# Optimization experiments

Measured on AMD Instinct MI355X. Metric: run time of the kernel, lower is better.

## Reference

```python
import jax, jax.numpy as jnp
from jax import lax
import numpy as np

G, K = 8, 9  # deformable groups, 3x3 kernel taps


def conv1x1_bn_relu(x, W, scale, bias):
    # Conv2d 1x1 (no bias) + folded eval-mode BatchNorm (per-channel scale/bias) + ReLU
    y = jnp.einsum('bchw,oc->bohw', x, W)
    return jax.nn.relu(y * scale[None, :, None, None] + bias[None, :, None, None])


def dcn_v2(feat, offset_feat, W_om, b_om, W_dcn, b_dcn):
    # Modulated deformable conv v2, 3x3, stride 1, pad 1, dilation 1,
    # deformable_groups=G, extra_offset_mask: offsets/mask predicted from offset_feat.
    B, C, H, W_ = feat.shape
    Cg = C // G
    om = lax.conv_general_dilated(offset_feat, W_om, (1, 1), ((1, 1), (1, 1)))
    om = om + b_om[None, :, None, None]              # [B, 3*G*K, H, W]
    o1, o2, m = jnp.split(om, 3, axis=1)
    off_y = o1.reshape(B, G, K, H, W_)
    off_x = o2.reshape(B, G, K, H, W_)
    mask = jax.nn.sigmoid(m).reshape(B, G, K, H, W_)
    dk = jnp.arange(3) - 1
    dkh = jnp.repeat(dk, 3)   # tap row offset,  k = kh*3 + kw
    dkw = jnp.tile(dk, 3)     # tap col offset
    hh = jnp.arange(H, dtype=feat.dtype)
    ww = jnp.arange(W_, dtype=feat.dtype)
    py = hh[None, None, None, :, None] + dkh[None, None, :, None, None].astype(feat.dtype) + off_y
    px = ww[None, None, None, None, :] + dkw[None, None, :, None, None].astype(feat.dtype) + off_x
    y0 = jnp.floor(py); x0 = jnp.floor(px)
    ty = py - y0; tx = px - x0
    xg = feat.reshape(B, G, Cg, H * W_)

    def gather(idx):  # idx [B,G,K,H,W] int32 -> [B,G,Cg,K,H,W]
        f = lambda xf, i: xf[:, i]
        return jax.vmap(jax.vmap(f))(xg, idx)

    val = jnp.zeros((B, G, Cg, K, H, W_), dtype=feat.dtype)
    y0i = y0.astype(jnp.int32); x0i = x0.astype(jnp.int32)
    for dy, wy in ((0, 1.0 - ty), (1, ty)):
        iy = y0i + dy
        vy = (iy >= 0) & (iy < H)
        iyc = jnp.clip(iy, 0, H - 1)
        for dx, wx in ((0, 1.0 - tx), (1, tx)):
            ix = x0i + dx
            v = vy & (ix >= 0) & (ix < W_)
            idx = iyc * W_ + jnp.clip(ix, 0, W_ - 1)
            w = (wy * wx) * v.astype(feat.dtype)      # zero-padding outside
            val = val + w[:, :, None] * gather(idx)
    val = val * mask[:, :, None]                      # modulation
    Wd = W_dcn.reshape(W_dcn.shape[0], G, Cg, K)      # [Cout, G, Cg, K]
    out = jnp.einsum('bgckhw,ogck->bohw', val, Wd) + b_dcn[None, :, None, None]
    return out


def setup_inputs() -> dict:
    key = jax.random.key(0)
    ks = jax.random.split(key, 16)
    B, C, H, W_ = 8, 128, 64, 64
    Cd = C // 2  # dcn out channels = 64
    d = {}
    d['feat_l'] = jax.random.normal(ks[0], (B, C, H, W_), jnp.float32)
    d['feat_s'] = jax.random.normal(ks[1], (B, C, H // 2, W_ // 2), jnp.float32)
    d['W_fsm'] = jax.random.normal(ks[2], (C, C), jnp.float32) / np.sqrt(C)
    d['s_fsm'] = 1.0 + 0.1 * jax.random.normal(ks[3], (C,), jnp.float32)
    d['b_fsm'] = 0.1 * jax.random.normal(ks[4], (C,), jnp.float32)
    d['W_off'] = jax.random.normal(ks[5], (C, 2 * C), jnp.float32) / np.sqrt(2 * C)
    d['s_off'] = 1.0 + 0.1 * jax.random.normal(ks[6], (C,), jnp.float32)
    d['b_off'] = 0.1 * jax.random.normal(ks[7], (C,), jnp.float32)
    d['W_om'] = 0.05 * jax.random.normal(ks[8], (3 * G * K, C, 3, 3), jnp.float32)
    d['b_om'] = jnp.zeros((3 * G * K,), jnp.float32)
    d['W_dcn'] = jax.random.normal(ks[9], (Cd, C, 3, 3), jnp.float32) / np.sqrt(C * 9)
    d['b_dcn'] = 0.1 * jax.random.normal(ks[10], (Cd,), jnp.float32)
    d['W_cat'] = jax.random.normal(ks[11], (C, Cd), jnp.float32) / np.sqrt(Cd)
    d['s_cat'] = 1.0 + 0.1 * jax.random.normal(ks[12], (C,), jnp.float32)
    d['b_cat'] = 0.1 * jax.random.normal(ks[13], (C,), jnp.float32)
    return d


def reference(feat_l, feat_s, W_fsm, s_fsm, b_fsm, W_off, s_off, b_off,
              W_om, b_om, W_dcn, b_dcn, W_cat, s_cat, b_cat):
    # nearest upsample x2 (F.interpolate nearest to feat_l spatial size)
    feat_up = jnp.repeat(jnp.repeat(feat_s, 2, axis=2), 2, axis=3)
    feat_arm = conv1x1_bn_relu(feat_l, W_fsm, s_fsm, b_fsm)
    offset = conv1x1_bn_relu(jnp.concatenate([feat_arm, feat_up * 2.0], axis=1),
                             W_off, s_off, b_off)
    feat_align = jax.nn.relu(dcn_v2(feat_up, offset, W_om, b_om, W_dcn, b_dcn))
    feat = conv1x1_bn_relu(feat_align, W_cat, s_cat, b_cat) + feat_arm
    return (feat, feat_arm)
```

## Files before the change

kernel.cpp:

```cpp
#include <hip/hip_runtime.h>


typedef __attribute__((ext_vector_type(8))) short short8;
typedef __attribute__((ext_vector_type(4))) float f32x4;
typedef __attribute__((ext_vector_type(16))) float f32x16;
typedef _Float16 __attribute__((ext_vector_type(2))) h2;

union F16u { f32x16 v; f32x4 q[4]; };

static __device__ __forceinline__ unsigned short f2bf(float x) {
    union { float f; unsigned int u; } v; v.f = x;
    return (unsigned short)((v.u + 0x7FFF + ((v.u >> 16) & 1)) >> 16);
}
static __device__ __forceinline__ unsigned short f2h(float x) {
    union { _Float16 h; unsigned short u; } v; v.h = (_Float16)x;
    return v.u;
}

__global__ __launch_bounds__(256) void k_prep(const float* __restrict__ fs,
        uint4* __restrict__ fsT4, uint4* __restrict__ fsC4,
        const float* __restrict__ W_fsm, const float* __restrict__ W_off,
        const float* __restrict__ W_cat, const float* __restrict__ W_dcn,
        const float* __restrict__ W_om,
        unsigned short* __restrict__ wbfsm, unsigned short* __restrict__ wboff,
        unsigned short* __restrict__ wbcat, unsigned short* __restrict__ wbdcn,
        unsigned short* __restrict__ wb2) {
    __shared__ unsigned short st[64 * 136];
    const int t = threadIdx.x;
    if (blockIdx.x < 128) {
        unsigned int* st32 = (unsigned int*)st;
        const int b = blockIdx.x >> 4;
        const int p0 = (blockIdx.x & 15) << 6;
        for (int i = t; i < 64 * 64; i += 256) {
            int c2 = i >> 6, px = i & 63;
            float v0 = fs[(((b << 7) + 2 * c2) << 10) + p0 + px];
            float v1 = fs[(((b << 7) + 2 * c2 + 1) << 10) + p0 + px];
            st32[px * 68 + c2] = (unsigned int)f2bf(v0) | ((unsigned int)f2bf(v1) << 16);
        }
        __syncthreads();
        for (int i = t; i < 64 * 16; i += 256) {
            int px = i >> 4, q = i & 15;
            fsT4[(((b << 10) + p0 + px) << 4) + q] = ((const uint4*)(st + px * 136))[q];
        }
        __syncthreads();
        for (int i = t; i < 64 * 64; i += 256) {
            int c2 = i >> 6, px = i & 63;
            float v0 = fs[(((b << 7) + 2 * c2) << 10) + p0 + px];
            float v1 = fs[(((b << 7) + 2 * c2 + 1) << 10) + p0 + px];
            st32[px * 68 + c2] = (unsigned int)f2h(v0) | ((unsigned int)f2h(v1) << 16);
        }
        __syncthreads();
        for (int i = t; i < 64 * 16; i += 256) {
            int ci = i >> 6, px = i & 63;
            fsC4[(b << 14) + (ci << 10) + p0 + px] = ((const uint4*)(st + px * 136))[ci];
        }
        return;
    }
    int idx = (blockIdx.x - 128) * 256 + t;
    int lane = idx & 63;
    int ml = lane & 15, kl = (lane >> 4) * 8;
    unsigned short tmp[8];
    if (idx < 2048) {
        int r = idx >> 6;
        int o = (r % 8) * 16 + ml, k0 = (r / 8) * 32 + kl;
#pragma unroll
        for (int j = 0; j < 8; j++) tmp[j] = f2bf(W_fsm[o * 128 + k0 + j]);
        ((uint4*)wbfsm)[idx] = *(const uint4*)tmp;
    } else if (idx < 6144) {
        int i2 = idx - 2048;
        int r = i2 >> 6;
        int o = (r % 8) * 16 + ml, k0 = (r / 8) * 32 + kl;
#pragma unroll
        for (int j = 0; j < 8; j++) {
            int k = k0 + j;
            float f = W_off[o * 256 + k];
            if (k >= 128) f *= 2.0f;
            tmp[j] = f2bf(f);
        }
        ((uint4*)wboff)[i2] = *(const uint4*)tmp;
    } else if (idx < 7168) {
        int i2 = idx - 6144;
        int r = i2 >> 6;
        int o = (r % 8) * 16 + ml, k0 = (r / 8) * 32 + kl;
#pragma unroll
        for (int j = 0; j < 8; j++) tmp[j] = f2bf(W_cat[o * 64 + k0 + j]);
        ((uint4*)wbcat)[i2] = *(const uint4*)tmp;
    } else if (idx < 16384) {
        int i2 = idx - 7168;
        int r = i2 >> 6;
        int o = (r & 1) * 32 + (lane & 31);
        int k0 = (r >> 1) * 16 + (lane >> 5) * 8;
#pragma unroll
        for (int j = 0; j < 8; j++) {
            int k = k0 + j;
            int g = k / 144;
            int rem = k - g * 144;
            tmp[j] = f2h(W_dcn[(o * 128 + g * 16 + (rem & 15)) * 9 + (rem >> 4)]);
        }
        ((uint4*)wbdcn)[i2] = *(const uint4*)tmp;
    } else if (idx < 48640) {
        int i2 = idx - 16384;
        int r = i2 >> 6;
        int nt = r % 14, kk = r / 14;
        int tap = kk >> 2, cc = kk & 3;
        int o = nt * 16 + ml;
        int c0 = cc * 32 + kl;
#pragma unroll
        for (int j = 0; j < 8; j++) {
            float v = (o < 216) ? W_om[(o * 128 + (c0 + j)) * 9 + tap] : 0.0f;
            tmp[j] = f2bf(v);
        }
        ((uint4*)wb2)[i2] = *(const uint4*)tmp;
    }
}

__global__ __launch_bounds__(512, 6) void k12(const float* __restrict__ feat_l,
        const uint4* __restrict__ fsT4,
        const unsigned short* __restrict__ wbf, const unsigned short* __restrict__ wbo,
        const float* __restrict__ s_fsm, const float* __restrict__ b_fsm,
        const float* __restrict__ s_off, const float* __restrict__ b_off,
        float* __restrict__ feat_arm, unsigned short* __restrict__ offT) {
    __shared__ unsigned short A1[64 * 136];
    __shared__ unsigned short A2[64 * 264];
    const int t = threadIdx.x;
    const int b = blockIdx.x >> 6;
    const int h = blockIdx.x & 63;
    const int hw0 = h << 6;
    unsigned int* A1w = (unsigned int*)A1;
    for (int i = t; i < 64 * 64; i += 512) {
        int c2 = i >> 6, px = i & 63;
        float v0 = feat_l[(((b << 7) + 2 * c2) << 12) + hw0 + px];
        float v1 = feat_l[(((b << 7) + 2 * c2 + 1) << 12) + hw0 + px];
        A1w[px * 68 + c2] = (unsigned int)f2bf(v0) | ((unsigned int)f2bf(v1) << 16);
    }
    {
        const int h2 = h >> 1;
        int px2 = t >> 4, q = t & 15;
        uint4 v = fsT4[(((b << 10) + (h2 << 5) + px2) << 4) + q];
        ((uint4*)(A2 + (2 * px2) * 264 + 128))[q] = v;
        ((uint4*)(A2 + (2 * px2 + 1) * 264 + 128))[q] = v;
    }
    __syncthreads();
    const int lane = t & 63;
    const int w = __builtin_amdgcn_readfirstlane(t >> 6);
    const int ph = w & 1;
    const int nq4 = w >> 1;
    const int m = lane & 15, ko = lane >> 4;
    f32x4 acc[2][2];
#pragma unroll
    for (int i = 0; i < 2; i++)
#pragma unroll
        for (int j = 0; j < 2; j++) acc[i][j] = (f32x4){0.f, 0.f, 0.f, 0.f};
#pragma unroll
    for (int kk = 0; kk < 4; kk++) {
        short8 a8[2];
#pragma unroll
        for (int mt = 0; mt < 2; mt++)
            a8[mt] = *(const short8*)(A1 + ((ph << 5) + (mt << 4) + m) * 136 + kk * 32 + ko * 8);
#pragma unroll
        for (int nt2 = 0; nt2 < 2; nt2++) {
            uint4 bu = ((const uint4*)wbf)[((kk << 3) + (nq4 << 1) + nt2) * 64 + lane];
#pragma unroll
            for (int mt = 0; mt < 2; mt++)
                acc[mt][nt2] = __builtin_amdgcn_mfma_f32_16x16x32_bf16(
                    a8[mt], *(short8*)&bu, acc[mt][nt2], 0, 0, 0);
        }
    }
#pragma unroll
    for (int nt2 = 0; nt2 < 2; nt2++) {
        int o = (((nq4 << 1) + nt2) << 4) + m;
        float sc = s_fsm[o], bi = b_fsm[o];
#pragma unroll
        for (int mt = 0; mt < 2; mt++) {
            int px0 = (ph << 5) + (mt << 4) + (ko << 2);
            f32x4 v;
#pragma unroll
            for (int r = 0; r < 4; r++) {
                float vv = fmaf(acc[mt][nt2][r], sc, bi);
                vv = vv > 0.f ? vv : 0.f;
                v[r] = vv;
                A2[(px0 + r) * 264 + o] = f2bf(vv);
            }
            *(f32x4*)(feat_arm + ((((b << 7) + o) << 12) + hw0 + px0)) = v;
        }
    }
    __syncthreads();
    f32x4 acc2[2][2];
#pragma unroll
    for (int i = 0; i < 2; i++)
#pragma unroll
        for (int j = 0; j < 2; j++) acc2[i][j] = (f32x4){0.f, 0.f, 0.f, 0.f};
#pragma unroll
    for (int kk = 0; kk < 8; kk++) {
        short8 a8[2];
#pragma unroll
        for (int mt = 0; mt < 2; mt++)
            a8[mt] = *(const short8*)(A2 + ((ph << 5) + (mt << 4) + m) * 264 + kk * 32 + ko * 8);
#pragma unroll
        for (int nt2 = 0; nt2 < 2; nt2++) {
            uint4 bu = ((const uint4*)wbo)[((kk << 3) + (nq4 << 1) + nt2) * 64 + lane];
#pragma unroll
            for (int mt = 0; mt < 2; mt++)
                acc2[mt][nt2] = __builtin_amdgcn_mfma_f32_16x16x32_bf16(
                    a8[mt], *(short8*)&bu, acc2[mt][nt2], 0, 0, 0);
        }
    }
    __syncthreads();
#pragma unroll
    for (int nt2 = 0; nt2 < 2; nt2++) {
        int o = (((nq4 << 1) + nt2) << 4) + m;
        float sc = s_off[o], bi = b_off[o];
#pragma unroll
        for (int mt = 0; mt < 2; mt++) {
            int px0 = (ph << 5) + (mt << 4) + (ko << 2);
#pragma unroll
            for (int r = 0; r < 4; r++) {
                float v = fmaf(acc2[mt][nt2][r], sc, bi);
                v = v > 0.f ? v : 0.f;
                A2[(px0 + r) * 264 + o] = f2bf(v);
            }
        }
    }
    __syncthreads();
    for (int i = t; i < 64 * 16; i += 512) {
        int px = i >> 4, q = i & 15;
        ((uint4*)offT)[(((b << 12) + hw0 + px) << 4) + q] = ((const uint4*)(A2 + px * 264))[q];
    }
}

__global__ __launch_bounds__(512, 4) void k_omdcn(
        const unsigned short* __restrict__ offT, const uint4* __restrict__ fsC4,
        const unsigned short* __restrict__ Wb2, const float* __restrict__ bom,
        const unsigned short* __restrict__ wbd, const float* __restrict__ bd,
        const unsigned short* __restrict__ wbc,
        const float* __restrict__ s_cat, const float* __restrict__ b_cat,
        const float* __restrict__ feat_arm, float* __restrict__ feat) {
    __shared__ float LDSf[13464];
    unsigned short* st = (unsigned short*)LDSf;
    float* oyL = LDSf;
    float* oxL = LDSf + 4672;
    unsigned short* mskL = (unsigned short*)(LDSf + 9344);
    float* Rbuf = LDSf;
    unsigned short* A3 = (unsigned short*)(LDSf + 9216);
    const uint4* offT4 = (const uint4*)offT;
    const uint4* W4 = (const uint4*)Wb2;
    const uint4* wbd4 = (const uint4*)wbd;
    const int t = threadIdx.x;
    const int b = blockIdx.x >> 6;
    const int h = blockIdx.x & 63;
    for (int i = t; i < 3 * 66 * 16; i += 512) {
        int q = i & 15;
        int rp = i >> 4;
        int r = rp / 66, p = rp - r * 66;
        int gy = h + r - 1, gx = p - 1;
        uint4 v = make_uint4(0, 0, 0, 0);
        if (gy >= 0 && gy < 64 && gx >= 0 && gx < 64)
            v = offT4[((((b << 6) + gy) << 6) + gx) * 16 + q];
        ((uint4*)(st + rp * 136))[q] = v;
    }
    __syncthreads();
    const int lane = t & 63;
    const int w = __builtin_amdgcn_readfirstlane(t >> 6);
    const int m = lane & 15, ko = lane >> 4;
    f32x4 acc[2][4];
#pragma unroll
    for (int i = 0; i < 2; i++)
#pragma unroll
        for (int j = 0; j < 4; j++) acc[i][j] = (f32x4){0.f, 0.f, 0.f, 0.f};
    if (w < 7) {
        const int ntb = w << 1;
        uint4 b4c[2];
#pragma unroll
        for (int nt2 = 0; nt2 < 2; nt2++)
            b4c[nt2] = W4[((ntb + nt2) << 6) + lane];
#pragma unroll
        for (int kk = 0; kk < 36; kk++) {
            const int tap = kk >> 2, cc = kk & 3;
            const int dy = tap / 3, dx = tap - dy * 3;
            uint4 b4n[2];
            if (kk < 35) {
#pragma unroll
                for (int nt2 = 0; nt2 < 2; nt2++)
                    b4n[nt2] = W4[(((kk + 1) * 14 + ntb + nt2) << 6) + lane];
            }
            short8 a8[4];
#pragma unroll
            for (int mt = 0; mt < 4; mt++) {
                int p = mt * 16 + m + dx;
                a8[mt] = *(const short8*)(st + (dy * 66 + p) * 136 + (cc << 5) + (ko << 3));
            }
            __builtin_amdgcn_s_setprio(1);
#pragma unroll
            for (int nt2 = 0; nt2 < 2; nt2++)
#pragma unroll
                for (int mt = 0; mt < 4; mt++)
                    acc[nt2][mt] = __builtin_amdgcn_mfma_f32_16x16x32_bf16(
                        a8[mt], *(short8*)&b4c[nt2], acc[nt2][mt], 0, 0, 0);
            __builtin_amdgcn_s_setprio(0);
            if (kk < 35) {
#pragma unroll
                for (int nt2 = 0; nt2 < 2; nt2++) b4c[nt2] = b4n[nt2];
            }
        }
    }
    __syncthreads();
    if (w < 7) {
#pragma unroll
        for (int nt2 = 0; nt2 < 2; nt2++) {
            int o = (((w << 1) + nt2) << 4) + m;
            if (o < 216) {
                float bv = bom[o];
#pragma unroll
                for (int mt = 0; mt < 4; mt++) {
                    f32x4 v = acc[nt2][mt];
#pragma unroll
                    for (int r = 0; r < 4; r++) {
                        int px = mt * 16 + (ko << 2) + r;
                        float val = v[r] + bv;
                        if (o < 72) {
                            oyL[px * 73 + o] = val;
                        } else if (o < 144) {
                            oxL[px * 73 + (o - 72)] = val;
                        } else {
                            float sg = 1.0f / (1.0f + __expf(-val));
                            mskL[px * 74 + (o - 144)] = f2h(sg);
                        }
                    }
                }
            }
        }
    }
    __syncthreads();
    const int p2 = w & 1;
    const int kq = w >> 1;
    const int oct = lane >> 5;
    const int l31 = lane & 31;
    const int px = (p2 << 5) + l31;
    const float fh = (float)h, fw = (float)px;
    const int b14 = b << 14;
    const float* oyrow = oyL + px * 73 + kq * 18;
    const float* oxrow = oxL + px * 73 + kq * 18;
    const unsigned short* mrow = mskL + px * 74 + kq * 18;
    const uint4* bp0 = fsC4 + b14 + (((kq << 2) + oct) << 10);
    const uint4* wbbase = wbd4 + (kq * 36) * 64 + lane;
    F16u acc3[2];
#pragma unroll
    for (int nt = 0; nt < 2; nt++)
#pragma unroll
        for (int q = 0; q < 4; q++) acc3[nt].q[q] = (f32x4){0.f, 0.f, 0.f, 0.f};
#pragma unroll
    for (int si = 0; si < 18; si++) {
        const int tap = si % 9;
        const int dy = tap / 3, dx = tap - dy * 3;
        float oy = oyrow[si];
        float ox = oxrow[si];
        float mmv = (float)(*(const _Float16*)(mrow + si));
        float py = fh + (float)(dy - 1) + oy;
        float pxx = fw + (float)(dx - 1) + ox;
        float y0f = floorf(py), x0f = floorf(pxx);
        float tyf = py - y0f, txf = pxx - x0f;
        int y0i = (int)y0f, x0i = (int)x0f;
        int y1i = y0i + 1, x1i = x0i + 1;
        bool vy0 = (y0i >= 0) && (y0i < 64);
        bool vy1 = (y1i >= 0) && (y1i < 64);
        bool vx0 = (x0i >= 0) && (x0i < 64);
        bool vx1 = (x1i >= 0) && (x1i < 64);
        float w00 = (vy0 && vx0) ? (1.0f - tyf) * (1.0f - txf) * mmv : 0.0f;
        float w01 = (vy0 && vx1) ? (1.0f - tyf) * txf * mmv : 0.0f;
        float w10 = (vy1 && vx0) ? tyf * (1.0f - txf) * mmv : 0.0f;
        float w11 = (vy1 && vx1) ? tyf * txf * mmv : 0.0f;
        int yc0 = y0i < 0 ? 0 : (y0i > 63 ? 63 : y0i);
        int yc1 = y1i < 0 ? 0 : (y1i > 63 ? 63 : y1i);
        int xc0 = x0i < 0 ? 0 : (x0i > 63 ? 63 : x0i);
        int xc1 = x1i < 0 ? 0 : (x1i > 63 ? 63 : x1i);
        int row0 = (yc0 >> 1) << 5, row1 = (yc1 >> 1) << 5;
        const uint4* bpp = (si < 9) ? bp0 : (bp0 + 2048);
        uint4 c00 = bpp[row0 + (xc0 >> 1)];
        uint4 c01 = bpp[row0 + (xc1 >> 1)];
        uint4 c10 = bpp[row1 + (xc0 >> 1)];
        uint4 c11 = bpp[row1 + (xc1 >> 1)];
        _Float16 h00 = (_Float16)w00, h01 = (_Float16)w01;
        _Float16 h10 = (_Float16)w10, h11 = (_Float16)w11;
        h2 W00 = (h2){h00, h00}, W01 = (h2){h01, h01};
        h2 W10 = (h2){h10, h10}, W11 = (h2){h11, h11};
        union { uint4 u; h2 h[4]; } U00, U01, U10, U11;
        U00.u = c00; U01.u = c01; U10.u = c10; U11.u = c11;
        union { short8 s; h2 h[4]; } av;
#pragma unroll
        for (int c = 0; c < 4; c++)
            av.h[c] = U00.h[c] * W00 + U01.h[c] * W01 + U10.h[c] * W10 + U11.h[c] * W11;
        uint4 bu0 = wbbase[(si * 2) * 64];
        uint4 bu1 = wbbase[(si * 2 + 1) * 64];
        __builtin_amdgcn_s_setprio(1);
        acc3[0].v = __builtin_amdgcn_mfma_f32_32x32x16_f16(av.s, *(short8*)&bu0, acc3[0].v, 0, 0, 0);
        acc3[1].v = __builtin_amdgcn_mfma_f32_32x32x16_f16(av.s, *(short8*)&bu1, acc3[1].v, 0, 0, 0);
        __builtin_amdgcn_s_setprio(0);
    }
    __syncthreads();
    if (kq >= 2) {
        float* rb = Rbuf + ((((kq - 2) << 1) + p2) * 64 + lane) * 36;
#pragma unroll
        for (int nt = 0; nt < 2; nt++)
#pragma unroll
            for (int q = 0; q < 4; q++)
                *(f32x4*)(rb + (nt << 4) + (q << 2)) = acc3[nt].q[q];
    }
    __syncthreads();
    if (kq < 2) {
        const float* rb = Rbuf + (((kq << 1) + p2) * 64 + lane) * 36;
#pragma unroll
        for (int nt = 0; nt < 2; nt++)
#pragma unroll
            for (int q = 0; q < 4; q++)
                acc3[nt].q[q] += *(const f32x4*)(rb + (nt << 4) + (q << 2));
    }
    __syncthreads();
    if (kq == 1) {
        float* rb = Rbuf + (p2 * 64 + lane) * 36;
#pragma unroll
        for (int nt = 0; nt < 2; nt++)
#pragma unroll
            for (int q = 0; q < 4; q++)
                *(f32x4*)(rb + (nt << 4) + (q << 2)) = acc3[nt].q[q];
    }
    __syncthreads();
    if (kq == 0) {
        const float* rb = Rbuf + (p2 * 64 + lane) * 36;
#pragma unroll
        for (int nt = 0; nt < 2; nt++)
#pragma unroll
            for (int q = 0; q < 4; q++)
                acc3[nt].q[q] += *(const f32x4*)(rb + (nt << 4) + (q << 2));
#pragma unroll
        for (int nt = 0; nt < 2; nt++) {
            int o = (nt << 5) + l31;
            float bv = bd[o];
#pragma unroll
            for (int r = 0; r < 16; r++) {
                int rowm = (r & 3) + ((r >> 2) << 3) + (oct << 2);
                float v = acc3[nt].v[r] + bv;
                v = v > 0.f ? v : 0.f;
                A3[((p2 << 5) + rowm) * 72 + o] = f2bf(v);
            }
        }
    }
    __syncthreads();
    const int nq = w & 3;
    const int kh = w >> 2;
    f32x4 acc2[4];
#pragma unroll
    for (int nt2 = 0; nt2 < 4; nt2++) acc2[nt2] = (f32x4){0.f, 0.f, 0.f, 0.f};
#pragma unroll
    for (int kk2 = 0; kk2 < 2; kk2++) {
        short8 av = *(const short8*)(A3 + ((nq << 4) + m) * 72 + kk2 * 32 + (ko << 3));
#pragma unroll
        for (int nt2 = 0; nt2 < 4; nt2++) {
            uint4 bu = ((const uint4*)wbc)[(kk2 * 8 + (kh << 2) + nt2) * 64 + lane];
            acc2[nt2] = __builtin_amdgcn_mfma_f32_16x16x32_bf16(av, *(short8*)&bu, acc2[nt2], 0, 0, 0);
        }
    }
    {
        const int px0 = (nq << 4) + (ko << 2);
        const int base = (b << 19) + (h << 6) + px0;
        f32x4 fa[4];
#pragma unroll
        for (int nt2 = 0; nt2 < 4; nt2++) {
            int o = (((kh << 2) + nt2) << 4) + m;
            fa[nt2] = *(const f32x4*)(feat_arm + base + (o << 12));
        }
#pragma unroll
        for (int nt2 = 0; nt2 < 4; nt2++) {
            int o = (((kh << 2) + nt2) << 4) + m;
            float sc = s_cat[o], bi = b_cat[o];
            f32x4 v;
#pragma unroll
            for (int r = 0; r < 4; r++) {
                float vv = fmaf(acc2[nt2][r], sc, bi);
                vv = vv > 0.f ? vv : 0.f;
                v[r] = vv + fa[nt2][r];
            }
            *(f32x4*)(feat + base + (o << 12)) = v;
        }
    }
}

extern "C" void kernel_launch(void* const* d_in, const int* in_sizes, int n_in,
                              void* d_out, int out_size, void* d_ws, size_t ws_size,
                              hipStream_t stream) {
    const float* feat_l = (const float*)d_in[0];
    const float* feat_s = (const float*)d_in[1];
    const float* W_fsm  = (const float*)d_in[2];
    const float* s_fsm  = (const float*)d_in[3];
    const float* b_fsm  = (const float*)d_in[4];
    const float* W_off  = (const float*)d_in[5];
    const float* s_off  = (const float*)d_in[6];
    const float* b_off  = (const float*)d_in[7];
    const float* W_om   = (const float*)d_in[8];
    const float* b_om   = (const float*)d_in[9];
    const float* W_dcn  = (const float*)d_in[10];
    const float* b_dcn  = (const float*)d_in[11];
    const float* W_cat  = (const float*)d_in[12];
    const float* s_cat  = (const float*)d_in[13];
    const float* b_cat  = (const float*)d_in[14];

    float* feat     = (float*)d_out;
    float* feat_arm = feat + 4194304;

    float* ws = (float*)d_ws;
    unsigned short* offT = (unsigned short*)ws;
    uint4* fsT4  = (uint4*)(ws + 9175040);
    unsigned short* wb2   = (unsigned short*)(ws + 9699328);
    unsigned short* wbfsm = (unsigned short*)(ws + 9846784);
    unsigned short* wboff = (unsigned short*)(ws + 9854976);
    unsigned short* wbcat = (unsigned short*)(ws + 9871360);
    unsigned short* wbdcn = (unsigned short*)(ws + 9875456);
    uint4* fsC4  = (uint4*)(ws + 9912320);

    k_prep<<<318, 256, 0, stream>>>(feat_s, fsT4, fsC4, W_fsm, W_off, W_cat,
                                    W_dcn, W_om, wbfsm, wboff, wbcat, wbdcn, wb2);

    k12<<<512, 512, 0, stream>>>(feat_l, fsT4, wbfsm, wboff,
                                 s_fsm, b_fsm, s_off, b_off, feat_arm, offT);
    k_omdcn<<<512, 512, 0, stream>>>(offT, fsC4, wb2, b_om, wbdcn, b_dcn,
                                     wbcat, s_cat, b_cat, feat_arm, feat);
}
```

Measured before the change: 155.6 us.

## Split fused offset/DCN kernel into half-row blocks to double grid and occupancy

The fused offset-mask conv plus DCN plus 1x1 conv kernel now processes 32 pixels (half a row) per block instead of 64. The grid doubles to 1024 blocks and LDS shrinks, allowing launch bounds of 8 blocks per SM. The DCN work split changes from 2 pixel halves x 4 tap groups to 8 wave-level group splits, with a deeper 3-stage LDS reduction tree. The aim is more parallelism and latency hiding, at the cost of extra halo reloads of offset features, more reduction syncs, and a tighter register budget.

```diff
diff --git a/kernel.cpp b/kernel.cpp
--- a/kernel.cpp
+++ b/kernel.cpp
@@ -228,31 +228,33 @@
     }
 }
 
-__global__ __launch_bounds__(512, 4) void k_omdcn(
+__global__ __launch_bounds__(512, 8) void k_omdcn(
         const unsigned short* __restrict__ offT, const uint4* __restrict__ fsC4,
         const unsigned short* __restrict__ Wb2, const float* __restrict__ bom,
         const unsigned short* __restrict__ wbd, const float* __restrict__ bd,
         const unsigned short* __restrict__ wbc,
         const float* __restrict__ s_cat, const float* __restrict__ b_cat,
         const float* __restrict__ feat_arm, float* __restrict__ feat) {
-    __shared__ float LDSf[13464];
+    __shared__ float LDSf[9216];
     unsigned short* st = (unsigned short*)LDSf;
     float* oyL = LDSf;
-    float* oxL = LDSf + 4672;
-    unsigned short* mskL = (unsigned short*)(LDSf + 9344);
+    float* oxL = LDSf + 2336;
+    unsigned short* mskL = (unsigned short*)(LDSf + 4672);
     float* Rbuf = LDSf;
-    unsigned short* A3 = (unsigned short*)(LDSf + 9216);
+    unsigned short* A3 = (unsigned short*)(LDSf + 6912);
     const uint4* offT4 = (const uint4*)offT;
     const uint4* W4 = (const uint4*)Wb2;
     const uint4* wbd4 = (const uint4*)wbd;
     const int t = threadIdx.x;
-    const int b = blockIdx.x >> 6;
-    const int h = blockIdx.x & 63;
-    for (int i = t; i < 3 * 66 * 16; i += 512) {
+    const int b = blockIdx.x >> 7;
+    const int h = (blockIdx.x >> 1) & 63;
+    const int xh = blockIdx.x & 1;
+    const int px0 = xh << 5;
+    for (int i = t; i < 3 * 34 * 16; i += 512) {
         int q = i & 15;
         int rp = i >> 4;
-        int r = rp / 66, p = rp - r * 66;
-        int gy = h + r - 1, gx = p - 1;
+        int r = rp / 34, p = rp - r * 34;
+        int gy = h + r - 1, gx = px0 + p - 1;
         uint4 v = make_uint4(0, 0, 0, 0);
         if (gy >= 0 && gy < 64 && gx >= 0 && gx < 64)
             v = offT4[((((b << 6) + gy) << 6) + gx) * 16 + q];
@@ -262,11 +264,11 @@
     const int lane = t & 63;
     const int w = __builtin_amdgcn_readfirstlane(t >> 6);
     const int m = lane & 15, ko = lane >> 4;
-    f32x4 acc[2][4];
+    f32x4 acc[2][2];
 #pragma unroll
     for (int i = 0; i < 2; i++)
 #pragma unroll
-        for (int j = 0; j < 4; j++) acc[i][j] = (f32x4){0.f, 0.f, 0.f, 0.f};
+        for (int j = 0; j < 2; j++) acc[i][j] = (f32x4){0.f, 0.f, 0.f, 0.f};
     if (w < 7) {
         const int ntb = w << 1;
         uint4 b4c[2];
@@ -283,17 +285,17 @@
                 for (int nt2 = 0; nt2 < 2; nt2++)
                     b4n[nt2] = W4[(((kk + 1) * 14 + ntb + nt2) << 6) + lane];
             }
-            short8 a8[4];
-#pragma unroll
-            for (int mt = 0; mt < 4; mt++) {
+            short8 a8[2];
+#pragma unroll
+            for (int mt = 0; mt < 2; mt++) {
                 int p = mt * 16 + m + dx;
-                a8[mt] = *(const short8*)(st + (dy * 66 + p) * 136 + (cc << 5) + (ko << 3));
+                a8[mt] = *(const short8*)(st + (dy * 34 + p) * 136 + (cc << 5) + (ko << 3));
             }
             __builtin_amdgcn_s_setprio(1);
 #pragma unroll
             for (int nt2 = 0; nt2 < 2; nt2++)
 #pragma unroll
-                for (int mt = 0; mt < 4; mt++)
+                for (int mt = 0; mt < 2; mt++)
                     acc[nt2][mt] = __builtin_amdgcn_mfma_f32_16x16x32_bf16(
                         a8[mt], *(short8*)&b4c[nt2], acc[nt2][mt], 0, 0, 0);
             __builtin_amdgcn_s_setprio(0);
@@ -311,7 +313,7 @@
             if (o < 216) {
                 float bv = bom[o];
 #pragma unroll
-                for (int mt = 0; mt < 4; mt++) {
+                for (int mt = 0; mt < 2; mt++) {
                     f32x4 v = acc[nt2][mt];
 #pragma unroll
                     for (int r = 0; r < 4; r++) {
@@ -331,27 +333,22 @@
         }
     }
     __syncthreads();
-    const int p2 = w & 1;
-    const int kq = w >> 1;
     const int oct = lane >> 5;
     const int l31 = lane & 31;
-    const int px = (p2 << 5) + l31;
-    const float fh = (float)h, fw = (float)px;
-    const int b14 = b << 14;
-    const float* oyrow = oyL + px * 73 + kq * 18;
-    const float* oxrow = oxL + px * 73 + kq * 18;
-    const unsigned short* mrow = mskL + px * 74 + kq * 18;
-    const uint4* bp0 = fsC4 + b14 + (((kq << 2) + oct) << 10);
-    const uint4* wbbase = wbd4 + (kq * 36) * 64 + lane;
+    const float fh = (float)h, fw = (float)(px0 + l31);
+    const float* oyrow = oyL + l31 * 73 + w * 9;
+    const float* oxrow = oxL + l31 * 73 + w * 9;
+    const unsigned short* mrow = mskL + l31 * 74 + w * 9;
+    const uint4* bp0 = fsC4 + (b << 14) + (((w << 1) + oct) << 10);
+    const uint4* wbbase = wbd4 + (w * 18) * 64 + lane;
     F16u acc3[2];
 #pragma unroll
     for (int nt = 0; nt < 2; nt++)
 #pragma unroll
         for (int q = 0; q < 4; q++) acc3[nt].q[q] = (f32x4){0.f, 0.f, 0.f, 0.f};
 #pragma unroll
-    for (int si = 0; si < 18; si++) {
-        const int tap = si % 9;
-        const int dy = tap / 3, dx = tap - dy * 3;
+    for (int si = 0; si < 9; si++) {
+        const int dy = si / 3, dx = si - dy * 3;
         float oy = oyrow[si];
         float ox = oxrow[si];
         float mmv = (float)(*(const _Float16*)(mrow + si));
@@ -374,11 +371,10 @@
         int xc0 = x0i < 0 ? 0 : (x0i > 63 ? 63 : x0i);
         int xc1 = x1i < 0 ? 0 : (x1i > 63 ? 63 : x1i);
         int row0 = (yc0 >> 1) << 5, row1 = (yc1 >> 1) << 5;
-        const uint4* bpp = (si < 9) ? bp0 : (bp0 + 2048);
-        uint4 c00 = bpp[row0 + (xc0 >> 1)];
-        uint4 c01 = bpp[row0 + (xc1 >> 1)];
-        uint4 c10 = bpp[row1 + (xc0 >> 1)];
-        uint4 c11 = bpp[row1 + (xc1 >> 1)];
+        uint4 c00 = bp0[row0 + (xc0 >> 1)];
+        uint4 c01 = bp0[row0 + (xc1 >> 1)];
+        uint4 c10 = bp0[row1 + (xc0 >> 1)];
+        uint4 c11 = bp0[row1 + (xc1 >> 1)];
         _Float16 h00 = (_Float16)w00, h01 = (_Float16)w01;
         _Float16 h10 = (_Float16)w10, h11 = (_Float16)w11;
         h2 W00 = (h2){h00, h00}, W01 = (h2){h01, h01};
@@ -397,8 +393,8 @@
         __builtin_amdgcn_s_setprio(0);
     }
     __syncthreads();
-    if (kq >= 2) {
-        float* rb = Rbuf + ((((kq - 2) << 1) + p2) * 64 + lane) * 36;
+    if (w >= 4) {
+        float* rb = Rbuf + ((w - 4) * 64 + lane) * 36;
 #pragma unroll
         for (int nt = 0; nt < 2; nt++)
 #pragma unroll
@@ -406,8 +402,8 @@
                 *(f32x4*)(rb + (nt << 4) + (q << 2)) = acc3[nt].q[q];
     }
     __syncthreads();
-    if (kq < 2) {
-        const float* rb = Rbuf + (((kq << 1) + p2) * 64 + lane) * 36;
+    if (w < 4) {
+        const float* rb = Rbuf + (w * 64 + lane) * 36;
 #pragma unroll
         for (int nt = 0; nt < 2; nt++)
 #pragma unroll
@@ -415,8 +411,8 @@
                 acc3[nt].q[q] += *(const f32x4*)(rb + (nt << 4) + (q << 2));
     }
     __syncthreads();
-    if (kq == 1) {
-        float* rb = Rbuf + (p2 * 64 + lane) * 36;
+    if (w == 2 || w == 3) {
+        float* rb = Rbuf + ((w - 2) * 64 + lane) * 36;
 #pragma unroll
         for (int nt = 0; nt < 2; nt++)
 #pragma unroll
@@ -424,8 +420,26 @@
                 *(f32x4*)(rb + (nt << 4) + (q << 2)) = acc3[nt].q[q];
     }
     __syncthreads();
-    if (kq == 0) {
-        const float* rb = Rbuf + (p2 * 64 + lane) * 36;
+    if (w < 2) {
+        const float* rb = Rbuf + (w * 64 + lane) * 36;
+#pragma unroll
+        for (int nt = 0; nt < 2; nt++)
+#pragma unroll
+            for (int q = 0; q < 4; q++)
+                acc3[nt].q[q] += *(const f32x4*)(rb + (nt << 4) + (q << 2));
+    }
+    __syncthreads();
+    if (w == 1) {
+        float* rb = Rbuf + lane * 36;
+#pragma unroll
+        for (int nt = 0; nt < 2; nt++)
+#pragma unroll
+            for (int q = 0; q < 4; q++)
+                *(f32x4*)(rb + (nt << 4) + (q << 2)) = acc3[nt].q[q];
+    }
+    __syncthreads();
+    if (w == 0) {
+        const float* rb = Rbuf + lane * 36;
 #pragma unroll
         for (int nt = 0; nt < 2; nt++)
 #pragma unroll
@@ -440,46 +454,38 @@
                 int rowm = (r & 3) + ((r >> 2) << 3) + (oct << 2);
                 float v = acc3[nt].v[r] + bv;
                 v = v > 0.f ? v : 0.f;
-                A3[((p2 << 5) + rowm) * 72 + o] = f2bf(v);
-            }
-        }
-    }
-    __syncthreads();
-    const int nq = w & 3;
-    const int kh = w >> 2;
-    f32x4 acc2[4];
-#pragma unroll
-    for (int nt2 = 0; nt2 < 4; nt2++) acc2[nt2] = (f32x4){0.f, 0.f, 0.f, 0.f};
+                A3[rowm * 72 + o] = f2bf(v);
+            }
+        }
+    }
+    __syncthreads();
+    f32x4 acc2[2];
+#pragma unroll
+    for (int mt = 0; mt < 2; mt++) acc2[mt] = (f32x4){0.f, 0.f, 0.f, 0.f};
 #pragma unroll
     for (int kk2 = 0; kk2 < 2; kk2++) {
-        short8 av = *(const short8*)(A3 + ((nq << 4) + m) * 72 + kk2 * 32 + (ko << 3));
-#pragma unroll
-        for (int nt2 = 0; nt2 < 4; nt2++) {
-            uint4 bu = ((const uint4*)wbc)[(kk2 * 8 + (kh << 2) + nt2) * 64 + lane];
-            acc2[nt2] = __builtin_amdgcn_mfma_f32_16x16x32_bf16(av, *(short8*)&bu, acc2[nt2], 0, 0, 0);
+        uint4 bu = ((const uint4*)wbc)[((kk2 << 3) + w) * 64 + lane];
+#pragma unroll
+        for (int mt = 0; mt < 2; mt++) {
+            short8 av = *(const short8*)(A3 + ((mt << 4) + m) * 72 + kk2 * 32 + (ko << 3));
+            acc2[mt] = __builtin_amdgcn_mfma_f32_16x16x32_bf16(av, *(short8*)&bu, acc2[mt], 0, 0, 0);
         }
     }
     {
-        const int px0 = (nq << 4) + (ko << 2);
-        const int base = (b << 19) + (h << 6) + px0;
-        f32x4 fa[4];
-#pragma unroll
-        for (int nt2 = 0; nt2 < 4; nt2++) {
-            int o = (((kh << 2) + nt2) << 4) + m;
-            fa[nt2] = *(const f32x4*)(feat_arm + base + (o << 12));
-        }
-#pragma unroll
-        for (int nt2 = 0; nt2 < 4; nt2++) {
-            int o = (((kh << 2) + nt2) << 4) + m;
-            float sc = s_cat[o], bi = b_cat[o];
+        int o = (w << 4) + m;
+        float sc = s_cat[o], bi = b_cat[o];
+#pragma unroll
+        for (int mt = 0; mt < 2; mt++) {
+            int gidx = (b << 19) + (o << 12) + (h << 6) + px0 + (mt << 4) + (ko << 2);
+            f32x4 fa = *(const f32x4*)(feat_arm + gidx);
             f32x4 v;
 #pragma unroll
             for (int r = 0; r < 4; r++) {
-                float vv = fmaf(acc2[nt2][r], sc, bi);
+                float vv = fmaf(acc2[mt][r], sc, bi);
                 vv = vv > 0.f ? vv : 0.f;
-                v[r] = vv + fa[nt2][r];
-            }
-            *(f32x4*)(feat + base + (o << 12)) = v;
+                v[r] = vv + fa[r];
+            }
+            *(f32x4*)(feat + gidx) = v;
         }
     }
 }
@@ -521,6 +527,6 @@
 
     k12<<<512, 512, 0, stream>>>(feat_l, fsT4, wbfsm, wboff,
                                  s_fsm, b_fsm, s_off, b_off, feat_arm, offT);
-    k_omdcn<<<512, 512, 0, stream>>>(offT, fsC4, wb2, b_om, wbdcn, b_dcn,
-                                     wbcat, s_cat, b_cat, feat_arm, feat);
+    k_omdcn<<<1024, 512, 0, stream>>>(offT, fsC4, wb2, b_om, wbdcn, b_dcn,
+                                      wbcat, s_cat, b_cat, feat_arm, feat);
 }
```

After: 259.4 us. +66.7%, slower.
